# Kernel tuning notes

Hardware: AMD Instinct MI355X
Metric: run time of the kernel (lower is better)

The kernel has to match this reference:

```python
import jax, jax.numpy as jnp
import numpy as np
from jax import lax

N, R, W, H = 256, 32, 8, 6       # batch, n_rooms, room width/height
MX, MY = 72, 72                  # map grid
EMB = 6                          # room embedding width
CIN = 10 + EMB                   # conv input channels


def _boundaries(m):
    # m: [R, W, H] binary room masks -> [R, 4, W, H] (left, right, up, down edges)
    left = jnp.concatenate([m[:, :1, :], jnp.clip(m[:, 1:, :] - m[:, :-1, :], 0)], axis=1)
    right = jnp.concatenate([jnp.clip(m[:, :-1, :] - m[:, 1:, :], 0), m[:, -1:, :]], axis=1)
    up = jnp.concatenate([m[:, :, :1], jnp.clip(m[:, :, 1:] - m[:, :, :-1], 0)], axis=2)
    down = jnp.concatenate([jnp.clip(m[:, :, :-1] - m[:, :, 1:], 0), m[:, :, -1:]], axis=2)
    return jnp.stack([left, right, up, down], axis=1)


def setup_inputs() -> dict:
    key = jax.random.key(0)
    ks = jax.random.split(key, 12)
    room_map = (jax.random.uniform(ks[0], (R, W, H)) < 0.7).astype(jnp.float32)
    room_map = room_map.at[:, 0, 0].set(1.0)  # guarantee nonempty rooms
    doors = (jax.random.uniform(ks[1], (R, 4, W, H)) < 0.15).astype(jnp.float32) * room_map[:, None]
    room_tensor = jnp.concatenate([room_map[:, None], doors, _boundaries(room_map)], axis=1)  # [R,9,W,H]
    px = jax.random.randint(ks[2], (N, R), 0, MX - W)
    py = jax.random.randint(ks[3], (N, R), 0, MY - H)
    room_positions = jnp.stack([px, py], axis=-1).astype(jnp.int32)  # [N,R,2]

    def rn(k, shape, fan_in):
        return jax.random.normal(k, shape, jnp.float32) / np.float32(np.sqrt(fan_in))

    inp = dict(room_positions=room_positions, room_tensor=room_tensor)
    inp['room_embedding'] = jax.random.normal(ks[4], (R, EMB), jnp.float32)
    inp['w_conv1'] = rn(ks[5], (64, CIN, 5, 5), CIN * 25); inp['b_conv1'] = jnp.zeros((64,), jnp.float32)
    inp['w_conv2'] = rn(ks[6], (64, 64, 3, 3), 64 * 9);    inp['b_conv2'] = jnp.zeros((64,), jnp.float32)
    inp['w_conv3'] = rn(ks[7], (64, 64, 3, 3), 64 * 9);    inp['b_conv3'] = jnp.zeros((64,), jnp.float32)
    inp['w_room1'] = rn(ks[8], (128, 64), 64);   inp['b_room1'] = jnp.zeros((128,), jnp.float32)
    inp['w_room2'] = rn(ks[9], (128, 128), 128); inp['b_room2'] = jnp.zeros((128,), jnp.float32)
    inp['w_fc1'] = rn(ks[10], (256, 128), 128);  inp['b_fc1'] = jnp.zeros((256,), jnp.float32)
    inp['w_fc2'] = rn(ks[11], (256, 256), 256);  inp['b_fc2'] = jnp.zeros((256,), jnp.float32)
    return inp


def _conv2d_relu(x, w, b):
    pad = w.shape[-1] // 2
    y = lax.conv_general_dilated(x, w, (1, 1), [(pad, pad), (pad, pad)],
                                 dimension_numbers=('NCHW', 'OIHW', 'NCHW'))
    return jax.nn.relu(y + b[None, :, None, None])


def _forward(room_positions, room_tensor, room_embedding,
             w_conv1, b_conv1, w_conv2, b_conv2, w_conv3, b_conv3,
             w_room1, b_room1, w_room2, b_room2, w_fc1, b_fc1, w_fc2, b_fc2):
    room_map = room_tensor[:, 0]                      # [R,W,H]
    px = room_positions[..., 0]                       # [N,R]
    py = room_positions[..., 1]
    # ---- encode_map: scatter-add all rooms into grid ----
    bidx = jnp.arange(N)[:, None, None, None, None]
    cidx = jnp.arange(9)[None, None, :, None, None]
    ix = px[:, :, None, None, None] + jnp.arange(W)[None, None, None, :, None]   # [N,R,1,W,1]
    iy = py[:, :, None, None, None] + jnp.arange(H)[None, None, None, None, :]   # [N,R,1,1,H]
    map9 = jnp.zeros((N, 9, MX, MY), jnp.float32).at[bidx, cidx, ix, iy].add(room_tensor[None])
    eidx = jnp.arange(EMB)[None, None, :, None, None]
    evals = room_embedding[:, :, None, None] * room_map[:, None, :, :]           # [R,EMB,W,H]
    embg = jnp.zeros((N, EMB, MX, MY), jnp.float32).at[bidx, eidx, ix, iy].add(evals[None])
    X = jnp.concatenate([map9, jnp.ones((N, 1, MX, MY), jnp.float32), embg], axis=1)  # [N,16,MX,MY]
    # ---- map convs ----
    X = _conv2d_relu(X, w_conv1, b_conv1)
    X = _conv2d_relu(X, w_conv2, b_conv2)
    X = _conv2d_relu(X, w_conv3, b_conv3)
    # ---- decode_map: gather room tiles, masked mean per room ----
    Xt = jnp.transpose(X, (0, 2, 3, 1))                                          # [N,MX,MY,C]
    g = Xt[jnp.arange(N)[:, None, None, None],
           px[:, :, None, None] + jnp.arange(W)[None, None, :, None],
           py[:, :, None, None] + jnp.arange(H)[None, None, None, :]]            # [N,R,W,H,C]
    g = g * room_map[None, :, :, :, None]
    room_feat = g.sum(axis=(2, 3)) / room_map.sum(axis=(1, 2))[None, :, None]    # [N,R,C]
    X = jnp.transpose(room_feat, (0, 2, 1))                                      # [N,C,R]
    # ---- 1x1 conv1d room layers ----
    X = jax.nn.relu(jnp.einsum('ncr,oc->nor', X, w_room1) + b_room1[None, :, None])
    X = jax.nn.relu(jnp.einsum('ncr,oc->nor', X, w_room2) + b_room2[None, :, None])
    # ---- fc head: sum over rooms, MLP ----
    X = X.sum(axis=2)                                                            # [N,128]
    X = jax.nn.relu(X @ w_fc1.T + b_fc1)
    return X @ w_fc2.T + b_fc2                                                   # [N,256]


def reference(room_positions, room_tensor, room_embedding,
              w_conv1, b_conv1, w_conv2, b_conv2, w_conv3, b_conv3,
              w_room1, b_room1, w_room2, b_room2, w_fc1, b_fc1, w_fc2, b_fc2):
    return _forward(room_positions, room_tensor, room_embedding,
                    w_conv1, b_conv1, w_conv2, b_conv2, w_conv3, b_conv3,
                    w_room1, b_room1, w_room2, b_room2, w_fc1, b_fc1, w_fc2, b_fc2)
```

## Files before the change

kernel.cpp:

```cpp
#include <hip/hip_runtime.h>
#include <hip/hip_bf16.h>
#include <cstddef>

#define NB 256
#define RR 32
#define WW 8
#define HH 6
#define MXY 72
#define EMB 6
#define CIN1 16

typedef __bf16 bf16x8 __attribute__((ext_vector_type(8)));
typedef float floatx4 __attribute__((ext_vector_type(4)));

static const size_t B_W1F  = 0;
static const size_t B_W2F  = 57344;
static const size_t B_W3F  = 131072;
static const size_t B_RAUX = 204800;
static const size_t B_RINV = 205056;
static const size_t B_HEAD = 205312;
static const size_t F_WR1T = 0;
static const size_t F_WR2T = 8192;
static const size_t F_F1T  = 24576;
static const size_t F_F2T  = 57344;
static const size_t B_FEAT = 696832;
static const size_t B_IMSK = 2793984;

__device__ inline short f2b(float f) {
    unsigned u = __builtin_bit_cast(unsigned, f);
    unsigned r = (u + 0x7fffu + ((u >> 16) & 1u)) >> 16;
    return (short)r;
}

__global__ void prep_weights(const float* __restrict__ w1, const float* __restrict__ w2,
                             const float* __restrict__ w3, const float* __restrict__ wr1,
                             const float* __restrict__ wr2, const float* __restrict__ wf1,
                             const float* __restrict__ wf2, char* __restrict__ ws)
{
    short* W1F = (short*)(ws + B_W1F);
    short* W2F = (short*)(ws + B_W2F);
    short* W3F = (short*)(ws + B_W3F);
    float* HEAD = (float*)(ws + B_HEAD);

    int idx = blockIdx.x * 256 + threadIdx.x;
    if (idx < 28672) {
        int j = idx & 7, lane = (idx >> 3) & 63, nt = (idx >> 9) & 3, kk = idx >> 11;
        int k = kk * 32 + (lane >> 4) * 8 + j;
        int oc = nt * 16 + (lane & 15);
        int tap = k >> 4, ci = k & 15;
        float v = (tap < 25) ? w1[(oc * 16 + ci) * 25 + tap] : 0.f;
        W1F[idx] = f2b(v);
        return;
    }
    idx -= 28672;
    if (idx < 36864) {
        int j = idx & 7, lane = (idx >> 3) & 63, nt = (idx >> 9) & 3, kk = idx >> 11;
        int k = kk * 32 + (lane >> 4) * 8 + j;
        int oc = nt * 16 + (lane & 15);
        int tap = k >> 6, cp = k & 63;
        int ci = (cp >> 2) + (cp & 3) * 16;
        W2F[idx] = f2b(w2[(oc * 64 + ci) * 9 + tap]);
        return;
    }
    idx -= 36864;
    if (idx < 36864) {
        int j = idx & 7, lane = (idx >> 3) & 63, nt = (idx >> 9) & 3, kk = idx >> 11;
        int k = kk * 32 + (lane >> 4) * 8 + j;
        int oc = nt * 16 + (lane & 15);
        int tap = k >> 6, cp = k & 63;
        int ci = (cp >> 2) + (cp & 3) * 16;
        W3F[idx] = f2b(w3[(oc * 64 + ci) * 9 + tap]);
        return;
    }
    idx -= 36864;
    if (idx < 8192)  { int o = idx & 127, c = idx >> 7; HEAD[F_WR1T + idx] = wr1[o * 64 + c]; return; }
    idx -= 8192;
    if (idx < 16384) { int o = idx & 127, c = idx >> 7; HEAD[F_WR2T + idx] = wr2[o * 128 + c]; return; }
    idx -= 16384;
    if (idx < 32768) { int o = idx & 255, c = idx >> 8; HEAD[F_F1T + idx] = wf1[o * 128 + c]; return; }
    idx -= 32768;
    if (idx < 65536) { int o = idx & 255, c = idx >> 8; HEAD[F_F2T + idx] = wf2[o * 256 + c]; return; }
}

__global__ void prep_rooms(const float* __restrict__ rt, char* __restrict__ ws)
{
    int r = threadIdx.x;
    if (r >= RR) return;
    unsigned long long m = 0ull;
    int cnt = 0;
    for (int j = 0; j < WW * HH; ++j)
        if (rt[r * 9 * 48 + j] != 0.f) { m |= (1ull << j); ++cnt; }
    ((unsigned long long*)(ws + B_RAUX))[r] = m;
    ((float*)(ws + B_RINV))[r] = 1.f / (float)cnt;
}

__global__ void prep_imask(const int* __restrict__ pos, unsigned* __restrict__ imask)
{
    const int n = blockIdx.x;
    const int r0 = threadIdx.x;
    const int px0 = pos[(n * RR + r0) * 2 + 0];
    const int py0 = pos[(n * RR + r0) * 2 + 1];
    unsigned m = 0;
    for (int r = 0; r < RR; ++r) {
        int rpx = pos[(n * RR + r) * 2 + 0];
        int rpy = pos[(n * RR + r) * 2 + 1];
        if (rpx >= px0 - 11 && rpx <= px0 + 11 && rpy >= py0 - 9 && rpy <= py0 + 9)
            m |= 1u << r;
    }
    imask[n * RR + r0] = m;
}

__global__ __launch_bounds__(256, 4) void fused_conv(
    const unsigned* __restrict__ imask, const float* __restrict__ rt,
    const float* __restrict__ emb, const short* __restrict__ wAll,
    const float* __restrict__ bc1, const float* __restrict__ bc2,
    const float* __restrict__ bc3, const int* __restrict__ pos,
    const unsigned long long* __restrict__ rmask, float* __restrict__ feat)
{
    __shared__ __align__(16) short s_Y1[120 * 72];
    __shared__ __align__(16) short s_u[80 * 72];
    __shared__ float s_feat[64];

    const int tid = threadIdx.x;
    const int lane = tid & 63;
    const int wv = tid >> 6;
    const int ml = lane & 15;
    const int q = lane >> 4;
    const int room = blockIdx.x;
    const int n = blockIdx.y;

    const int px = pos[(n * RR + room) * 2 + 0];
    const int py = pos[(n * RR + room) * 2 + 1];

    const short* W1F = wAll;
    const short* W2F = wAll + B_W2F / 2;
    const short* W3F = wAll + B_W3F / 2;

    bf16x8 Bb[2][4];
    auto load_k = [&](const short* wF, int kk, bf16x8* dst) {
        const short* src = wF + (size_t)kk * 2048;
#pragma unroll
        for (int j2 = 0; j2 < 4; ++j2)
            dst[j2] = *reinterpret_cast<const bf16x8*>(src + (j2 * 64 + lane) * 8);
    };

    load_k(W1F, 0, Bb[0]);

    {
        const unsigned mk0 = imask[n * RR + room];
        if (tid < 224) {
            const int row = tid / 14, col = tid - (tid / 14) * 14;
            const int gx = px - 4 + row, gy = py - 4 + col;
            float a[16];
#pragma unroll
            for (int c = 0; c < 16; ++c) a[c] = 0.f;
            a[9] = ((unsigned)gx < (unsigned)MXY && (unsigned)gy < (unsigned)MXY) ? 1.f : 0.f;

            unsigned mm = mk0;
            while (mm) {
                const int r = __builtin_ctz(mm);
                mm &= mm - 1;
                const int rpx = pos[(n * RR + r) * 2 + 0];
                const int rpy = pos[(n * RR + r) * 2 + 1];
                const int w = gx - rpx, h = gy - rpy;
                if ((unsigned)w < (unsigned)WW && (unsigned)h < (unsigned)HH) {
                    const int j = w * HH + h;
                    const float* rr = rt + r * 9 * 48;
#pragma unroll
                    for (int c = 0; c < 9; ++c) a[c] += rr[c * 48 + j];
                    const float mv = rr[j];
#pragma unroll
                    for (int e = 0; e < EMB; ++e) a[10 + e] += emb[r * EMB + e] * mv;
                }
            }
            short o[16];
#pragma unroll
            for (int c = 0; c < 16; ++c) o[c] = f2b(a[c]);
            *reinterpret_cast<uint4*>(&s_u[tid * 24 + 0]) = *reinterpret_cast<uint4*>(o);
            *reinterpret_cast<uint4*>(&s_u[tid * 24 + 8]) = *reinterpret_cast<uint4*>(o + 8);
        }
    }
    __syncthreads();

    {
        int prow[2], pcol[2];
#pragma unroll
        for (int i = 0; i < 2; ++i) {
            int p = wv * 32 + i * 16 + ml;
            if (p > 119) p = 119;
            prow[i] = p / 10; pcol[i] = p - prow[i] * 10;
        }
        floatx4 acc1[2][4] = {};

#pragma unroll
        for (int kk = 0; kk < 13; ++kk) {
            if (kk < 12) load_k(W1F, kk + 1, Bb[(kk + 1) & 1]);
            else         load_k(W2F, 0, Bb[1]);
            int tap = kk * 2 + (q >> 1);
            if (tap > 24) tap = 24;
            int chb = (q & 1) * 8;
            int dx = tap / 5, dy = tap - dx * 5;
            __builtin_amdgcn_s_setprio(1);
#pragma unroll
            for (int i = 0; i < 2; ++i) {
                bf16x8 A = *reinterpret_cast<const bf16x8*>(
                    &s_u[((prow[i] + dx) * 14 + (pcol[i] + dy)) * 24 + chb]);
#pragma unroll
                for (int j2 = 0; j2 < 4; ++j2)
                    acc1[i][j2] = __builtin_amdgcn_mfma_f32_16x16x32_bf16(
                        A, Bb[kk & 1][j2], acc1[i][j2], 0, 0, 0);
            }
            __builtin_amdgcn_s_setprio(0);
        }
        float b4[4];
#pragma unroll
        for (int j2 = 0; j2 < 4; ++j2) b4[j2] = bc1[j2 * 16 + ml];
#pragma unroll
        for (int i = 0; i < 2; ++i)
#pragma unroll
            for (int r = 0; r < 4; ++r) {
                int p = wv * 32 + i * 16 + q * 4 + r;
                if (p < 120) {
                    unsigned lo = (unsigned)(unsigned short)f2b(fmaxf(acc1[i][0][r] + b4[0], 0.f))
                                | ((unsigned)(unsigned short)f2b(fmaxf(acc1[i][1][r] + b4[1], 0.f)) << 16);
                    unsigned hi = (unsigned)(unsigned short)f2b(fmaxf(acc1[i][2][r] + b4[2], 0.f))
                                | ((unsigned)(unsigned short)f2b(fmaxf(acc1[i][3][r] + b4[3], 0.f)) << 16);
                    *reinterpret_cast<uint2*>(&s_Y1[p * 72 + ml * 4]) = make_uint2(lo, hi);
                }
            }
    }
    __syncthreads();

    {
        int prowA, pcolA, prowB, pcolB;
        {
            int p0 = wv * 16 + ml; prowA = p0 >> 3; pcolA = p0 & 7;
            int p1 = 64 + ml;      prowB = p1 >> 3; pcolB = p1 & 7;
        }
        floatx4 acc2[4] = {};
        floatx4 acc2s = {};

#pragma unroll
        for (int kk = 0; kk < 18; ++kk) {
            if (kk < 17) load_k(W2F, kk + 1, Bb[kk & 1]);
            else         load_k(W3F, 0, Bb[1]);
            bf16x8 B4 = *reinterpret_cast<const bf16x8*>(
                W2F + (size_t)kk * 2048 + (wv * 64 + lane) * 8);
            const int tap = kk >> 1;
            const int chb = (kk & 1) * 32 + q * 8;
            const int dx = tap / 3, dy = tap - (tap / 3) * 3;
            bf16x8 A0 = *reinterpret_cast<const bf16x8*>(
                &s_Y1[((prowA + dx) * 10 + (pcolA + dy)) * 72 + chb]);
            bf16x8 A4 = *reinterpret_cast<const bf16x8*>(
                &s_Y1[((prowB + dx) * 10 + (pcolB + dy)) * 72 + chb]);
            __builtin_amdgcn_s_setprio(1);
#pragma unroll
            for (int j2 = 0; j2 < 4; ++j2)
                acc2[j2] = __builtin_amdgcn_mfma_f32_16x16x32_bf16(A0, Bb[(kk + 1) & 1][j2], acc2[j2], 0, 0, 0);
            acc2s = __builtin_amdgcn_mfma_f32_16x16x32_bf16(A4, B4, acc2s, 0, 0, 0);
            __builtin_amdgcn_s_setprio(0);
        }
        float b4[4];
#pragma unroll
        for (int j2 = 0; j2 < 4; ++j2) b4[j2] = bc2[j2 * 16 + ml];
#pragma unroll
        for (int r = 0; r < 4; ++r) {
            int p = wv * 16 + q * 4 + r;
            unsigned lo = (unsigned)(unsigned short)f2b(fmaxf(acc2[0][r] + b4[0], 0.f))
                        | ((unsigned)(unsigned short)f2b(fmaxf(acc2[1][r] + b4[1], 0.f)) << 16);
            unsigned hi = (unsigned)(unsigned short)f2b(fmaxf(acc2[2][r] + b4[2], 0.f))
                        | ((unsigned)(unsigned short)f2b(fmaxf(acc2[3][r] + b4[3], 0.f)) << 16);
            *reinterpret_cast<uint2*>(&s_u[p * 72 + ml * 4]) = make_uint2(lo, hi);
        }
        {
            float bt = bc2[wv * 16 + ml];
#pragma unroll
            for (int r = 0; r < 4; ++r) {
                int p = 64 + q * 4 + r;
                s_u[p * 72 + ml * 4 + wv] = f2b(fmaxf(acc2s[r] + bt, 0.f));
            }
        }
        if (tid < 64) s_feat[tid] = 0.f;
    }
    __syncthreads();

    if (wv < 3) {
        int p0 = wv * 16 + ml;
        int row3 = p0 / 6, col3 = p0 - (p0 / 6) * 6;
        floatx4 acc3[4] = {};

#pragma unroll
        for (int kk = 0; kk < 18; ++kk) {
            if (kk < 17) load_k(W3F, kk + 1, Bb[kk & 1]);
            const int tap = kk >> 1;
            const int chb = (kk & 1) * 32 + q * 8;
            const int dx = tap / 3, dy = tap - (tap / 3) * 3;
            bf16x8 A = *reinterpret_cast<const bf16x8*>(
                &s_u[((row3 + dx) * 8 + (col3 + dy)) * 72 + chb]);
            __builtin_amdgcn_s_setprio(1);
#pragma unroll
            for (int j2 = 0; j2 < 4; ++j2)
                acc3[j2] = __builtin_amdgcn_mfma_f32_16x16x32_bf16(A, Bb[(kk + 1) & 1][j2], acc3[j2], 0, 0, 0);
            __builtin_amdgcn_s_setprio(0);
        }
        float b4[4];
#pragma unroll
        for (int j2 = 0; j2 < 4; ++j2) b4[j2] = bc3[j2 * 16 + ml];
        float part[4] = {0.f, 0.f, 0.f, 0.f};
        const unsigned long long mk = rmask[room];
#pragma unroll
        for (int r = 0; r < 4; ++r) {
            int p = wv * 16 + q * 4 + r;
            if ((mk >> p) & 1ull) {
#pragma unroll
                for (int j2 = 0; j2 < 4; ++j2)
                    part[j2] += fmaxf(acc3[j2][r] + b4[j2], 0.f);
            }
        }
#pragma unroll
        for (int j2 = 0; j2 < 4; ++j2) {
            part[j2] += __shfl_xor(part[j2], 16);
            part[j2] += __shfl_xor(part[j2], 32);
        }
        if (q == 0) {
#pragma unroll
            for (int j2 = 0; j2 < 4; ++j2)
                atomicAdd(&s_feat[j2 * 16 + ml], part[j2]);
        }
    }
    __syncthreads();
    if (tid < 64)
        feat[((size_t)n * RR + room) * 64 + tid] = s_feat[tid];
}

__global__ __launch_bounds__(256) void mlp_head(const float* __restrict__ feat,
                                                const float* __restrict__ HEAD,
                                                const float* __restrict__ rinv,
                                                const float* __restrict__ b1,
                                                const float* __restrict__ b2,
                                                const float* __restrict__ bf1,
                                                const float* __restrict__ bf2,
                                                float* __restrict__ outp)
{
    __shared__ __align__(16) float s_feat[RR * 64];
    __shared__ __align__(16) float s_h1[RR * 128];
    __shared__ __align__(16) float s_s[2 * 128];
    __shared__ __align__(16) float s_sf[128];
    __shared__ __align__(16) float s_t1[256];

    const int n = blockIdx.x;
    const int tid = threadIdx.x;
    const float* W1t = HEAD + F_WR1T;
    const float* W2t = HEAD + F_WR2T;
    const float* F1t = HEAD + F_F1T;
    const float* F2t = HEAD + F_F2T;

    for (int i = tid; i < RR * 64; i += 256)
        s_feat[i] = feat[(size_t)n * RR * 64 + i] * rinv[i >> 6];
    __syncthreads();

    const int o = tid & 127;
    const int rh = tid >> 7;

    float acc[16];
#pragma unroll
    for (int r = 0; r < 16; ++r) acc[r] = b1[o];
    for (int c4 = 0; c4 < 16; ++c4) {
        float w0 = W1t[(c4 * 4 + 0) * 128 + o];
        float w1 = W1t[(c4 * 4 + 1) * 128 + o];
        float w2 = W1t[(c4 * 4 + 2) * 128 + o];
        float w3 = W1t[(c4 * 4 + 3) * 128 + o];
#pragma unroll
        for (int r = 0; r < 16; ++r) {
            float4 f = *reinterpret_cast<const float4*>(&s_feat[(rh * 16 + r) * 64 + c4 * 4]);
            acc[r] += f.x * w0 + f.y * w1 + f.z * w2 + f.w * w3;
        }
    }
#pragma unroll
    for (int r = 0; r < 16; ++r) s_h1[(rh * 16 + r) * 128 + o] = fmaxf(acc[r], 0.f);
    __syncthreads();

#pragma unroll
    for (int r = 0; r < 16; ++r) acc[r] = b2[o];
    for (int c4 = 0; c4 < 32; ++c4) {
        float w0 = W2t[(c4 * 4 + 0) * 128 + o];
        float w1 = W2t[(c4 * 4 + 1) * 128 + o];
        float w2 = W2t[(c4 * 4 + 2) * 128 + o];
        float w3 = W2t[(c4 * 4 + 3) * 128 + o];
#pragma unroll
        for (int r = 0; r < 16; ++r) {
            float4 f = *reinterpret_cast<const float4*>(&s_h1[(rh * 16 + r) * 128 + c4 * 4]);
            acc[r] += f.x * w0 + f.y * w1 + f.z * w2 + f.w * w3;
        }
    }
    float ps = 0.f;
#pragma unroll
    for (int r = 0; r < 16; ++r) ps += fmaxf(acc[r], 0.f);
    s_s[rh * 128 + o] = ps;
    __syncthreads();
    if (tid < 128) s_sf[tid] = s_s[tid] + s_s[128 + tid];
    __syncthreads();

    {
        float a = bf1[tid];
        for (int c4 = 0; c4 < 32; ++c4) {
            float4 f = *reinterpret_cast<const float4*>(&s_sf[c4 * 4]);
            a += f.x * F1t[(c4 * 4 + 0) * 256 + tid];
            a += f.y * F1t[(c4 * 4 + 1) * 256 + tid];
            a += f.z * F1t[(c4 * 4 + 2) * 256 + tid];
            a += f.w * F1t[(c4 * 4 + 3) * 256 + tid];
        }
        s_t1[tid] = fmaxf(a, 0.f);
    }
    __syncthreads();

    {
        float a = bf2[tid];
        for (int c4 = 0; c4 < 64; ++c4) {
            float4 f = *reinterpret_cast<const float4*>(&s_t1[c4 * 4]);
            a += f.x * F2t[(c4 * 4 + 0) * 256 + tid];
            a += f.y * F2t[(c4 * 4 + 1) * 256 + tid];
            a += f.z * F2t[(c4 * 4 + 2) * 256 + tid];
            a += f.w * F2t[(c4 * 4 + 3) * 256 + tid];
        }
        outp[(size_t)n * 256 + tid] = a;
    }
}

extern "C" void kernel_launch(void* const* d_in, const int* in_sizes, int n_in,
                              void* d_out, int out_size, void* d_ws, size_t ws_size,
                              hipStream_t stream)
{
    const int* pos = (const int*)d_in[0];
    const float* rt = (const float*)d_in[1];
    const float* emb = (const float*)d_in[2];
    const float* w1 = (const float*)d_in[3];
    const float* bc1 = (const float*)d_in[4];
    const float* w2 = (const float*)d_in[5];
    const float* bc2 = (const float*)d_in[6];
    const float* w3 = (const float*)d_in[7];
    const float* bc3 = (const float*)d_in[8];
    const float* wr1 = (const float*)d_in[9];
    const float* br1 = (const float*)d_in[10];
    const float* wr2 = (const float*)d_in[11];
    const float* br2 = (const float*)d_in[12];
    const float* wf1 = (const float*)d_in[13];
    const float* bf1 = (const float*)d_in[14];
    const float* wf2 = (const float*)d_in[15];
    const float* bf2 = (const float*)d_in[16];
    float* out = (float*)d_out;
    char* ws = (char*)d_ws;

    prep_weights<<<880, 256, 0, stream>>>(w1, w2, w3, wr1, wr2, wf1, wf2, ws);
    prep_rooms<<<1, 64, 0, stream>>>(rt, ws);

    const short* WALL = (const short*)(ws + B_W1F);
    const unsigned long long* RMASK = (const unsigned long long*)(ws + B_RAUX);
    const float* RINV = (const float*)(ws + B_RINV);
    float* HEAD = (float*)(ws + B_HEAD);
    float* FEAT = (float*)(ws + B_FEAT);
    unsigned* IMSK = (unsigned*)(ws + B_IMSK);

    prep_imask<<<NB, RR, 0, stream>>>(pos, IMSK);

    fused_conv<<<dim3(RR, NB), 256, 0, stream>>>(IMSK, rt, emb, WALL,
                                                 bc1, bc2, bc3, pos, RMASK, FEAT);

    mlp_head<<<NB, 256, 0, stream>>>(FEAT, HEAD, RINV, br1, br2, bf1, bf2, out);
}
```

Measured before the change: 312.1 us.

## Merge prep kernels into one launch and raise fused_conv occupancy hint

Folds the room-mask and interaction-mask prep kernels into the weight-prep kernel by extending its flat index space, which cuts two kernel launches and their serialization gaps. It also changes fused_conv launch bounds from 4 to 5 waves per EU so more blocks can be resident. The higher occupancy target may force register spills in the conv kernel.

Measured after the change: 313.9 us. Within noise of the previous version (+0.6%).

```diff
diff --git a/kernel.cpp b/kernel.cpp
--- a/kernel.cpp
+++ b/kernel.cpp
@@ -32,10 +32,11 @@
     return (short)r;
 }
 
-__global__ void prep_weights(const float* __restrict__ w1, const float* __restrict__ w2,
-                             const float* __restrict__ w3, const float* __restrict__ wr1,
-                             const float* __restrict__ wr2, const float* __restrict__ wf1,
-                             const float* __restrict__ wf2, char* __restrict__ ws)
+__global__ void prep_all(const float* __restrict__ w1, const float* __restrict__ w2,
+                         const float* __restrict__ w3, const float* __restrict__ wr1,
+                         const float* __restrict__ wr2, const float* __restrict__ wf1,
+                         const float* __restrict__ wf2, const float* __restrict__ rt,
+                         const int* __restrict__ pos, char* __restrict__ ws)
 {
     short* W1F = (short*)(ws + B_W1F);
     short* W2F = (short*)(ws + B_W2F);
@@ -80,37 +81,33 @@
     if (idx < 32768) { int o = idx & 255, c = idx >> 8; HEAD[F_F1T + idx] = wf1[o * 128 + c]; return; }
     idx -= 32768;
     if (idx < 65536) { int o = idx & 255, c = idx >> 8; HEAD[F_F2T + idx] = wf2[o * 256 + c]; return; }
+    idx -= 65536;
+    if (idx < 8192) {
+        const int n = idx >> 5, r0 = idx & 31;
+        const int px0 = pos[(n * RR + r0) * 2 + 0];
+        const int py0 = pos[(n * RR + r0) * 2 + 1];
+        unsigned m = 0;
+        for (int r = 0; r < RR; ++r) {
+            int rpx = pos[(n * RR + r) * 2 + 0];
+            int rpy = pos[(n * RR + r) * 2 + 1];
+            if (rpx >= px0 - 11 && rpx <= px0 + 11 && rpy >= py0 - 9 && rpy <= py0 + 9)
+                m |= 1u << r;
+        }
+        ((unsigned*)(ws + B_IMSK))[n * RR + r0] = m;
+        return;
+    }
+    idx -= 8192;
+    if (idx < RR) {
+        unsigned long long m = 0ull;
+        int cnt = 0;
+        for (int j = 0; j < WW * HH; ++j)
+            if (rt[idx * 9 * 48 + j] != 0.f) { m |= (1ull << j); ++cnt; }
+        ((unsigned long long*)(ws + B_RAUX))[idx] = m;
+        ((float*)(ws + B_RINV))[idx] = 1.f / (float)cnt;
+    }
 }
 
-__global__ void prep_rooms(const float* __restrict__ rt, char* __restrict__ ws)
-{
-    int r = threadIdx.x;
-    if (r >= RR) return;
-    unsigned long long m = 0ull;
-    int cnt = 0;
-    for (int j = 0; j < WW * HH; ++j)
-        if (rt[r * 9 * 48 + j] != 0.f) { m |= (1ull << j); ++cnt; }
-    ((unsigned long long*)(ws + B_RAUX))[r] = m;
-    ((float*)(ws + B_RINV))[r] = 1.f / (float)cnt;
-}
-
-__global__ void prep_imask(const int* __restrict__ pos, unsigned* __restrict__ imask)
-{
-    const int n = blockIdx.x;
-    const int r0 = threadIdx.x;
-    const int px0 = pos[(n * RR + r0) * 2 + 0];
-    const int py0 = pos[(n * RR + r0) * 2 + 1];
-    unsigned m = 0;
-    for (int r = 0; r < RR; ++r) {
-        int rpx = pos[(n * RR + r) * 2 + 0];
-        int rpy = pos[(n * RR + r) * 2 + 1];
-        if (rpx >= px0 - 11 && rpx <= px0 + 11 && rpy >= py0 - 9 && rpy <= py0 + 9)
-            m |= 1u << r;
-    }
-    imask[n * RR + r0] = m;
-}
-
-__global__ __launch_bounds__(256, 4) void fused_conv(
+__global__ __launch_bounds__(256, 5) void fused_conv(
     const unsigned* __restrict__ imask, const float* __restrict__ rt,
     const float* __restrict__ emb, const short* __restrict__ wAll,
     const float* __restrict__ bc1, const float* __restrict__ bc2,
@@ -451,8 +448,7 @@
     float* out = (float*)d_out;
     char* ws = (char*)d_ws;
 
-    prep_weights<<<880, 256, 0, stream>>>(w1, w2, w3, wr1, wr2, wf1, wf2, ws);
-    prep_rooms<<<1, 64, 0, stream>>>(rt, ws);
+    prep_all<<<913, 256, 0, stream>>>(w1, w2, w3, wr1, wr2, wf1, wf2, rt, pos, ws);
 
     const short* WALL = (const short*)(ws + B_W1F);
     const unsigned long long* RMASK = (const unsigned long long*)(ws + B_RAUX);
@@ -461,8 +457,6 @@
     float* FEAT = (float*)(ws + B_FEAT);
     unsigned* IMSK = (unsigned*)(ws + B_IMSK);
 
-    prep_imask<<<NB, RR, 0, stream>>>(pos, IMSK);
-
     fused_conv<<<dim3(RR, NB), 256, 0, stream>>>(IMSK, rt, emb, WALL,
                                                  bc1, bc2, bc3, pos, RMASK, FEAT);
 
```
